# Optimization experiments

Hardware: AMD Instinct MI355X
Metric: run time of the kernel (lower is better)

## Reference

```python
import jax, jax.numpy as jnp
import numpy as np

B, N, M = 4096, 128, 64
EPS_COS = 1e-8   # torch F.cosine_similarity default eps (clamp on norms)


def setup_inputs() -> dict:
    key = jax.random.key(0)
    ks = jax.random.split(key, 7)
    stdev = 1.0 / np.sqrt(N + M)
    # reset(): memory = abs(randn(N, M).repeat(B,1,1) * stdev); we draw per-batch which is equivalent math-wise
    memory = jnp.abs(jax.random.normal(ks[0], (B, N, M), jnp.float32) * stdev)
    k = jax.random.normal(ks[1], (B, M), jnp.float32)
    beta = jax.random.normal(ks[2], (B, 1), jnp.float32)
    g = jax.random.normal(ks[3], (B, 1), jnp.float32)
    s = jax.random.normal(ks[4], (B, 3), jnp.float32)
    gamma = jax.random.normal(ks[5], (B, 1), jnp.float32)
    # w_prev is a weighting from the previous step: a valid distribution over N rows
    w_prev = jax.nn.softmax(jax.random.normal(ks[6], (B, N), jnp.float32), axis=1)
    return {"memory": memory, "k": k, "beta": beta, "g": g, "s": s,
            "gamma": gamma, "w_prev": w_prev}


def reference(memory, k, beta, g, s, gamma, w_prev):
    # parameter squashing (ROM.address)
    beta = jax.nn.softplus(beta)              # [B,1] key strength > 0
    g = jax.nn.sigmoid(g)                     # [B,1] interpolation gate
    s = jax.nn.softmax(s, axis=1)             # [B,3] shift weighting
    gamma = 1.0 + jax.nn.softplus(gamma)      # [B,1] sharpen >= 1

    # _similarity: cosine similarity between memory rows and key, then softmax
    mem = memory + 1e-16                      # [B,N,M]
    kk = k + 1e-16                            # [B,M]
    dot = jnp.einsum('bnm,bm->bn', mem, kk)   # [B,N]
    mem_norm = jnp.maximum(jnp.linalg.norm(mem, axis=-1), EPS_COS)            # [B,N]
    key_norm = jnp.maximum(jnp.linalg.norm(kk, axis=-1, keepdims=True), EPS_COS)  # [B,1]
    wc = jax.nn.softmax(beta * (dot / (mem_norm * key_norm)), axis=1)         # [B,N]

    # _interpolate
    wg = g * wc + (1.0 - g) * w_prev          # [B,N]

    # _shift: batched circular 3-tap convolution (replaces per-batch conv1d loop)
    # c[i] = w[(i-1)%N]*s[0] + w[i]*s[1] + w[(i+1)%N]*s[2]
    w_hat = (jnp.roll(wg, 1, axis=1) * s[:, 0:1]
             + wg * s[:, 1:2]
             + jnp.roll(wg, -1, axis=1) * s[:, 2:3])

    # _sharpen
    w = w_hat ** gamma
    return w / (jnp.sum(w, axis=1, keepdims=True) + 1e-16)
```

## Files before the change

kernel.cpp:

```cpp
#include <hip/hip_runtime.h>
#include <hip/hip_bf16.h>


constexpr int ROM_N = 128;
constexpr int ROM_M = 64;
constexpr int N_IN  = 7;
constexpr int PROW2 = 5;

typedef float  fx4 __attribute__((ext_vector_type(4)));
typedef unsigned int ux2 __attribute__((ext_vector_type(2)));

__device__ __forceinline__ float bf2f(unsigned short u) {
    union { unsigned int i; float f; } v;
    v.i = ((unsigned int)u) << 16;
    return v.f;
}

__device__ __forceinline__ unsigned short f2bf(float f) {
    union { float f; unsigned int i; } v; v.f = f;
    unsigned int x = v.i;
    x += 0x7fffu + ((x >> 16) & 1u);
    return (unsigned short)(x >> 16);
}

__device__ __forceinline__ float waveReduceSum(float v) {
#pragma unroll
    for (int off = 32; off > 0; off >>= 1) v += __shfl_down(v, off, 64);
    return v;
}

struct KArgs { const void* p[N_IN]; };

__device__ __forceinline__ float ld1(const void* p, size_t i, bool f32) {
    return f32 ? ((const float*)p)[i] : bf2f(((const unsigned short*)p)[i]);
}

__global__ __launch_bounds__(256) void rom_kernel(KArgs a, void* __restrict__ outp) {
    const int t    = threadIdx.x;
    const int h    = t >> 7;
    const int tt   = t & 127;
    const int b    = blockIdx.x * 2 + h;
    const int w    = t >> 6;
    const int wv   = w & 1;
    const int lane = t & 63;
    const int g16  = tt & 15;
    const int a16  = tt >> 4;

    __shared__ int    sf[2];
    __shared__ float  kk[2][ROM_M];
    __shared__ float  scal[2][6];
    __shared__ float  keynorm[2];
    __shared__ float  wreds[2][2], wredn[2][2];
    __shared__ float  wgs[2][ROM_N];
    __shared__ float2 part[2][ROM_N * PROW2];

    {
        int bad = 0;
        if (w < 2) {
            int j = t >> 4;
            if (j < N_IN) {
                ux2 q = ((const ux2*)a.p[j])[t & 15];
                unsigned int hw[4] = {q.x & 0xffffu, q.x >> 16,
                                      q.y & 0xffffu, q.y >> 16};
#pragma unroll
                for (int e = 0; e < 4; ++e) {
                    float v = bf2f((unsigned short)hw[e]);
                    if (!(fabsf(v) < 1e4f)) bad = 1;
                }
            }
        }
        unsigned long long mb = __ballot(bad);
        if (lane == 0 && w < 2) {
            int f = 0;
#pragma unroll
            for (int j4 = 0; j4 < 4; ++j4)
                if ((mb >> (16 * j4)) & 0xFFFFull) f |= 1 << (w * 4 + j4);
            sf[w] = f;
        }
    }
    __syncthreads();
    const int fm = sf[0] | sf[1];
    const bool memF32 = (fm >> 0) & 1, kF32 = (fm >> 1) & 1, beF32 = (fm >> 2) & 1;
    const bool gF32 = (fm >> 3) & 1, sF32 = (fm >> 4) & 1, gaF32 = (fm >> 5) & 1;
    const bool wpF32 = (fm >> 6) & 1;
    const bool outBf = (fm != 0x7F);

    if (tt < 64) {
        float kv = ld1(a.p[1], (size_t)b * ROM_M + tt, kF32) + 1e-16f;
        kk[h][tt] = kv;
        float ss = waveReduceSum(kv * kv);
        if (lane == 0) keynorm[h] = fmaxf(sqrtf(ss), 1e-8f);
    }
    if (tt == 64) {
        scal[h][0] = log1pf(expf(ld1(a.p[2], b, beF32)));
        scal[h][1] = 1.0f / (1.0f + expf(-ld1(a.p[3], b, gF32)));
        float s0 = ld1(a.p[4], (size_t)b * 3 + 0, sF32);
        float s1 = ld1(a.p[4], (size_t)b * 3 + 1, sF32);
        float s2 = ld1(a.p[4], (size_t)b * 3 + 2, sF32);
        float mx = fmaxf(s0, fmaxf(s1, s2));
        float e0 = expf(s0 - mx), e1 = expf(s1 - mx), e2 = expf(s2 - mx);
        float inv = 1.0f / (e0 + e1 + e2);
        scal[h][2] = e0 * inv; scal[h][3] = e1 * inv; scal[h][4] = e2 * inv;
        scal[h][5] = 1.0f + log1pf(expf(ld1(a.p[5], b, gaF32)));
    }
    float wp = ld1(a.p[6], (size_t)b * ROM_N + tt, wpF32);
    __syncthreads();

    const float4 kcv = ((const float4*)kk[h])[g16];
    float2* pp = part[h];
    const size_t mbase = (size_t)b * (ROM_N * ROM_M);
    if (memF32) {
        const fx4* mv = (const fx4*)((const float*)a.p[0] + mbase);
#pragma unroll
        for (int i = 0; i < 16; ++i) {
            fx4 v = __builtin_nontemporal_load(&mv[tt + 128 * i]);
            float a0 = v.x + 1e-16f, a1 = v.y + 1e-16f;
            float a2 = v.z + 1e-16f, a3 = v.w + 1e-16f;
            float d = a0 * kcv.x + a1 * kcv.y + a2 * kcv.z + a3 * kcv.w;
            float s = a0 * a0 + a1 * a1 + a2 * a2 + a3 * a3;
            d += __shfl_xor(d, 1); s += __shfl_xor(s, 1);
            d += __shfl_xor(d, 2); s += __shfl_xor(s, 2);
            if ((g16 & 3) == 0)
                pp[(a16 + 8 * i) * PROW2 + (g16 >> 2)] = make_float2(d, s);
        }
    } else {
        const ux2* mv = (const ux2*)((const unsigned short*)a.p[0] + mbase);
#pragma unroll
        for (int i = 0; i < 16; ++i) {
            ux2 u = __builtin_nontemporal_load(&mv[tt + 128 * i]);
            float a0 = bf2f((unsigned short)(u.x & 0xffffu)) + 1e-16f;
            float a1 = bf2f((unsigned short)(u.x >> 16)) + 1e-16f;
            float a2 = bf2f((unsigned short)(u.y & 0xffffu)) + 1e-16f;
            float a3 = bf2f((unsigned short)(u.y >> 16)) + 1e-16f;
            float d = a0 * kcv.x + a1 * kcv.y + a2 * kcv.z + a3 * kcv.w;
            float s = a0 * a0 + a1 * a1 + a2 * a2 + a3 * a3;
            d += __shfl_xor(d, 1); s += __shfl_xor(s, 1);
            d += __shfl_xor(d, 2); s += __shfl_xor(s, 2);
            if ((g16 & 3) == 0)
                pp[(a16 + 8 * i) * PROW2 + (g16 >> 2)] = make_float2(d, s);
        }
    }
    __syncthreads();

    float dot = 0.0f, ssq = 0.0f;
    const float2* pr = pp + tt * PROW2;
#pragma unroll
    for (int j = 0; j < 4; ++j) { float2 v = pr[j]; dot += v.x; ssq += v.y; }
    float mem_norm = fmaxf(sqrtf(ssq), 1e-8f);
    float x = scal[h][0] * (dot / (mem_norm * keynorm[h]));

    float e = __expf(x);
    float ps = waveReduceSum(e);
    if (lane == 0) wreds[h][wv] = ps;
    __syncthreads();
    float wc = e / (wreds[h][0] + wreds[h][1]);

    float g = scal[h][1];
    float wg = g * wc + (1.0f - g) * wp;
    wgs[h][tt] = wg;
    __syncthreads();

    float wh = wgs[h][(tt + ROM_N - 1) & (ROM_N - 1)] * scal[h][2]
             + wg * scal[h][3]
             + wgs[h][(tt + 1) & (ROM_N - 1)] * scal[h][4];

    float w2 = __expf(scal[h][5] * __logf(wh));
    float pn = waveReduceSum(w2);
    if (lane == 0) wredn[h][wv] = pn;
    __syncthreads();
    float val = w2 / (wredn[h][0] + wredn[h][1] + 1e-16f);

    const size_t oi = (size_t)b * ROM_N + tt;
    if (outBf) ((unsigned short*)outp)[oi] = f2bf(val);
    else       ((float*)outp)[oi] = val;
}

extern "C" void kernel_launch(void* const* d_in, const int* in_sizes, int n_in,
                              void* d_out, int out_size, void* d_ws, size_t ws_size,
                              hipStream_t stream) {
    KArgs a;
    for (int i = 0; i < N_IN; ++i) a.p[i] = d_in[i];
    const int B = in_sizes[0] / (ROM_N * ROM_M);
    rom_kernel<<<B / 2, 256, 0, stream>>>(a, d_out);
}
```

Measured before the change: 194.3 us.

## Prefetch memory tile before dtype sync and do softmax/shift tail with wave shuffles

Each wave now probes the memory dtype itself and issues all 16 memory loads into registers before the first block barrier, so global loads overlap the dtype-detection and scalar setup phases. The post-reduction tail is restructured so both waves of a batch redundantly compute all 128 entries (two per lane) using xor all-reduce and shuffles for the circular shift, removing three shared-memory barriers. This costs more registers (16 ux4 held live) and duplicated exp/log work, and leaves a dead duplicate probe block.

```diff
diff --git a/kernel.cpp b/kernel.cpp
--- a/kernel.cpp
+++ b/kernel.cpp
@@ -9,6 +9,7 @@
 
 typedef float  fx4 __attribute__((ext_vector_type(4)));
 typedef unsigned int ux2 __attribute__((ext_vector_type(2)));
+typedef unsigned int ux4 __attribute__((ext_vector_type(4)));
 
 __device__ __forceinline__ float bf2f(unsigned short u) {
     union { unsigned int i; float f; } v;
@@ -23,9 +24,9 @@
     return (unsigned short)(x >> 16);
 }
 
-__device__ __forceinline__ float waveReduceSum(float v) {
-#pragma unroll
-    for (int off = 32; off > 0; off >>= 1) v += __shfl_down(v, off, 64);
+__device__ __forceinline__ float waveAllSum(float v) {
+#pragma unroll
+    for (int off = 32; off > 0; off >>= 1) v += __shfl_xor(v, off, 64);
     return v;
 }
 
@@ -50,9 +51,49 @@
     __shared__ float  kk[2][ROM_M];
     __shared__ float  scal[2][6];
     __shared__ float  keynorm[2];
-    __shared__ float  wreds[2][2], wredn[2][2];
-    __shared__ float  wgs[2][ROM_N];
     __shared__ float2 part[2][ROM_N * PROW2];
+
+    {
+        int mbad = 0;
+        if (lane < 16) {
+            ux2 q = ((const ux2*)a.p[0])[lane];
+            unsigned int hw[4] = {q.x & 0xffffu, q.x >> 16,
+                                  q.y & 0xffffu, q.y >> 16};
+#pragma unroll
+            for (int e = 0; e < 4; ++e) {
+                float v = bf2f((unsigned short)hw[e]);
+                if (!(fabsf(v) < 1e4f)) mbad = 1;
+            }
+        }
+    }
+    int mbad = 0;
+    if (lane < 16) {
+        ux2 q = ((const ux2*)a.p[0])[lane];
+        unsigned int hw[4] = {q.x & 0xffffu, q.x >> 16,
+                              q.y & 0xffffu, q.y >> 16};
+#pragma unroll
+        for (int e = 0; e < 4; ++e) {
+            float v = bf2f((unsigned short)hw[e]);
+            if (!(fabsf(v) < 1e4f)) mbad = 1;
+        }
+    }
+    const bool memF32w = (__ballot(mbad) & 0xFFFFull) != 0ull;
+
+    const size_t mbase = (size_t)b * (ROM_N * ROM_M);
+    ux4 raw[16];
+    if (memF32w) {
+        const ux4* mv = (const ux4*)((const float*)a.p[0] + mbase);
+#pragma unroll
+        for (int i = 0; i < 16; ++i)
+            raw[i] = __builtin_nontemporal_load(&mv[tt + 128 * i]);
+    } else {
+        const ux2* mv = (const ux2*)((const unsigned short*)a.p[0] + mbase);
+#pragma unroll
+        for (int i = 0; i < 16; ++i) {
+            ux2 u = __builtin_nontemporal_load(&mv[tt + 128 * i]);
+            raw[i].x = u.x; raw[i].y = u.y;
+        }
+    }
 
     {
         int bad = 0;
@@ -80,7 +121,7 @@
     }
     __syncthreads();
     const int fm = sf[0] | sf[1];
-    const bool memF32 = (fm >> 0) & 1, kF32 = (fm >> 1) & 1, beF32 = (fm >> 2) & 1;
+    const bool kF32 = (fm >> 1) & 1, beF32 = (fm >> 2) & 1;
     const bool gF32 = (fm >> 3) & 1, sF32 = (fm >> 4) & 1, gaF32 = (fm >> 5) & 1;
     const bool wpF32 = (fm >> 6) & 1;
     const bool outBf = (fm != 0x7F);
@@ -88,7 +129,7 @@
     if (tt < 64) {
         float kv = ld1(a.p[1], (size_t)b * ROM_M + tt, kF32) + 1e-16f;
         kk[h][tt] = kv;
-        float ss = waveReduceSum(kv * kv);
+        float ss = waveAllSum(kv * kv);
         if (lane == 0) keynorm[h] = fmaxf(sqrtf(ss), 1e-8f);
     }
     if (tt == 64) {
@@ -103,19 +144,19 @@
         scal[h][2] = e0 * inv; scal[h][3] = e1 * inv; scal[h][4] = e2 * inv;
         scal[h][5] = 1.0f + log1pf(expf(ld1(a.p[5], b, gaF32)));
     }
-    float wp = ld1(a.p[6], (size_t)b * ROM_N + tt, wpF32);
+    float wp0 = ld1(a.p[6], (size_t)b * ROM_N + lane,      wpF32);
+    float wp1 = ld1(a.p[6], (size_t)b * ROM_N + 64 + lane, wpF32);
     __syncthreads();
 
     const float4 kcv = ((const float4*)kk[h])[g16];
     float2* pp = part[h];
-    const size_t mbase = (size_t)b * (ROM_N * ROM_M);
-    if (memF32) {
-        const fx4* mv = (const fx4*)((const float*)a.p[0] + mbase);
+    if (memF32w) {
 #pragma unroll
         for (int i = 0; i < 16; ++i) {
-            fx4 v = __builtin_nontemporal_load(&mv[tt + 128 * i]);
-            float a0 = v.x + 1e-16f, a1 = v.y + 1e-16f;
-            float a2 = v.z + 1e-16f, a3 = v.w + 1e-16f;
+            float a0 = __uint_as_float(raw[i].x) + 1e-16f;
+            float a1 = __uint_as_float(raw[i].y) + 1e-16f;
+            float a2 = __uint_as_float(raw[i].z) + 1e-16f;
+            float a3 = __uint_as_float(raw[i].w) + 1e-16f;
             float d = a0 * kcv.x + a1 * kcv.y + a2 * kcv.z + a3 * kcv.w;
             float s = a0 * a0 + a1 * a1 + a2 * a2 + a3 * a3;
             d += __shfl_xor(d, 1); s += __shfl_xor(s, 1);
@@ -124,14 +165,13 @@
                 pp[(a16 + 8 * i) * PROW2 + (g16 >> 2)] = make_float2(d, s);
         }
     } else {
-        const ux2* mv = (const ux2*)((const unsigned short*)a.p[0] + mbase);
 #pragma unroll
         for (int i = 0; i < 16; ++i) {
-            ux2 u = __builtin_nontemporal_load(&mv[tt + 128 * i]);
-            float a0 = bf2f((unsigned short)(u.x & 0xffffu)) + 1e-16f;
-            float a1 = bf2f((unsigned short)(u.x >> 16)) + 1e-16f;
-            float a2 = bf2f((unsigned short)(u.y & 0xffffu)) + 1e-16f;
-            float a3 = bf2f((unsigned short)(u.y >> 16)) + 1e-16f;
+            unsigned int ux = raw[i].x, uy = raw[i].y;
+            float a0 = bf2f((unsigned short)(ux & 0xffffu)) + 1e-16f;
+            float a1 = bf2f((unsigned short)(ux >> 16)) + 1e-16f;
+            float a2 = bf2f((unsigned short)(uy & 0xffffu)) + 1e-16f;
+            float a3 = bf2f((unsigned short)(uy >> 16)) + 1e-16f;
             float d = a0 * kcv.x + a1 * kcv.y + a2 * kcv.z + a3 * kcv.w;
             float s = a0 * a0 + a1 * a1 + a2 * a2 + a3 * a3;
             d += __shfl_xor(d, 1); s += __shfl_xor(s, 1);
@@ -142,35 +182,46 @@
     }
     __syncthreads();
 
-    float dot = 0.0f, ssq = 0.0f;
-    const float2* pr = pp + tt * PROW2;
-#pragma unroll
-    for (int j = 0; j < 4; ++j) { float2 v = pr[j]; dot += v.x; ssq += v.y; }
-    float mem_norm = fmaxf(sqrtf(ssq), 1e-8f);
-    float x = scal[h][0] * (dot / (mem_norm * keynorm[h]));
-
-    float e = __expf(x);
-    float ps = waveReduceSum(e);
-    if (lane == 0) wreds[h][wv] = ps;
-    __syncthreads();
-    float wc = e / (wreds[h][0] + wreds[h][1]);
-
-    float g = scal[h][1];
-    float wg = g * wc + (1.0f - g) * wp;
-    wgs[h][tt] = wg;
-    __syncthreads();
-
-    float wh = wgs[h][(tt + ROM_N - 1) & (ROM_N - 1)] * scal[h][2]
-             + wg * scal[h][3]
-             + wgs[h][(tt + 1) & (ROM_N - 1)] * scal[h][4];
-
-    float w2 = __expf(scal[h][5] * __logf(wh));
-    float pn = waveReduceSum(w2);
-    if (lane == 0) wredn[h][wv] = pn;
-    __syncthreads();
-    float val = w2 / (wredn[h][0] + wredn[h][1] + 1e-16f);
-
-    const size_t oi = (size_t)b * ROM_N + tt;
+    const float2* pr0 = pp + lane * PROW2;
+    const float2* pr1 = pp + (lane + 64) * PROW2;
+    float dot0 = 0.0f, ssq0 = 0.0f, dot1 = 0.0f, ssq1 = 0.0f;
+#pragma unroll
+    for (int j = 0; j < 4; ++j) {
+        float2 v0 = pr0[j]; dot0 += v0.x; ssq0 += v0.y;
+        float2 v1 = pr1[j]; dot1 += v1.x; ssq1 += v1.y;
+    }
+    const float beta = scal[h][0];
+    const float kn   = keynorm[h];
+    float x0 = beta * (dot0 / (fmaxf(sqrtf(ssq0), 1e-8f) * kn));
+    float x1 = beta * (dot1 / (fmaxf(sqrtf(ssq1), 1e-8f) * kn));
+
+    float e0 = __expf(x0), e1 = __expf(x1);
+    float inv_ps = 1.0f / waveAllSum(e0 + e1);
+
+    const float g = scal[h][1];
+    float wg0 = g * e0 * inv_ps + (1.0f - g) * wp0;
+    float wg1 = g * e1 * inv_ps + (1.0f - g) * wp1;
+
+    const int lm1 = (lane + 63) & 63, lp1 = (lane + 1) & 63;
+    float A  = __shfl(wg0, lm1, 64);
+    float Bv = __shfl(wg1, lm1, 64);
+    float C  = __shfl(wg0, lp1, 64);
+    float D  = __shfl(wg1, lp1, 64);
+    float prev0 = (lane == 0)  ? Bv : A;
+    float prev1 = (lane == 0)  ? A  : Bv;
+    float next0 = (lane == 63) ? D  : C;
+    float next1 = (lane == 63) ? C  : D;
+    const float s0v = scal[h][2], s1v = scal[h][3], s2v = scal[h][4];
+    float wh0 = prev0 * s0v + wg0 * s1v + next0 * s2v;
+    float wh1 = prev1 * s0v + wg1 * s1v + next1 * s2v;
+
+    const float ga = scal[h][5];
+    float W0 = __expf(ga * __logf(wh0));
+    float W1 = __expf(ga * __logf(wh1));
+    float inv_pn = 1.0f / (waveAllSum(W0 + W1) + 1e-16f);
+
+    float val = (wv == 0) ? W0 * inv_pn : W1 * inv_pn;
+    const size_t oi = (size_t)b * ROM_N + wv * 64 + lane;
     if (outBf) ((unsigned short*)outp)[oi] = f2bf(val);
     else       ((float*)outp)[oi] = val;
 }
```

Measured after the change: 199.3 us. 2.6% more time.
